# Kernel optimization log

Measured on AMD Instinct MI355X. Metric: run time of the kernel, lower is better.

Reference implementation:

```python
import jax, jax.numpy as jnp
import numpy as np
from jax.scipy.special import i0e

A = 10.0  # bessel concentration parameter (init kwarg a)


def setup_inputs() -> dict:
    key = jax.random.key(0)
    kx, ky = jax.random.split(key)
    x = jax.random.uniform(kx, (8192, 1), dtype=jnp.float32)
    y = jax.random.uniform(ky, (8192, 1), dtype=jnp.float32)
    return {"x": x, "y": y}


def reference(x, y):
    # K[i,j] = I0(2a*cos(pi*(x_i - y_j))) * exp(-2a)
    # Numerically stable form: I0(z)*exp(-2a) = i0e(z) * exp(|z| - 2a),
    # and |z| = |2a*cos(...)| <= 2a so the exponent is always <= 0.
    diff = x - y.T                      # [nx, ny]
    z = 2.0 * A * jnp.cos(jnp.pi * diff)
    return i0e(z) * jnp.exp(jnp.abs(z) - 2.0 * A)
```

## Files before the change

kernel.cpp:

```cpp
#include <hip/hip_runtime.h>
#include <hip/hip_bf16.h>


#define TWO_A 20.0f
#define EXP_NEG_2A 2.0611536224385578e-9f
#define LOG2E 1.4426950408889634f

__device__ __forceinline__ float bessel_elem(float xi, float yj) {
    float d = xi - yj;
#if __has_builtin(__builtin_amdgcn_cosf)
    float c = __builtin_amdgcn_cosf(0.5f * d);
#else
    float c = __cosf(3.14159265358979323846f * d);
#endif
    float az = TWO_A * fabsf(c);

    float t2 = az * (1.0f / 3.75f);
    t2 = t2 * t2;
    float ps = fmaf(t2, 0.0045813f, 0.0360768f);
    ps = fmaf(t2, ps, 0.2659732f);
    ps = fmaf(t2, ps, 1.2067492f);
    ps = fmaf(t2, ps, 3.0899424f);
    ps = fmaf(t2, ps, 3.5156229f);
    ps = fmaf(t2, ps, 1.0f);
    float k_small = ps * EXP_NEG_2A;

    float u = __fdividef(3.75f, az);
    float pl = fmaf(u, 0.00392377f, -0.01647633f);
    pl = fmaf(u, pl, 0.02635537f);
    pl = fmaf(u, pl, -0.02057706f);
    pl = fmaf(u, pl, 0.00916281f);
    pl = fmaf(u, pl, -0.00157565f);
    pl = fmaf(u, pl, 0.00225319f);
    pl = fmaf(u, pl, 0.01328592f);
    pl = fmaf(u, pl, 0.39894228f);
    float e = exp2f((az - TWO_A) * LOG2E);
    float k_large = pl * rsqrtf(az) * e;

    return (az < 3.75f) ? k_small : k_large;
}

__global__ __launch_bounds__(256) void bessel_kernel(
    const float* __restrict__ x, const float* __restrict__ y,
    float* __restrict__ out, int nx, int ny)
{
    const int i = blockIdx.y;
    const int j4 = (blockIdx.x * 256 + threadIdx.x) * 4;
    if (i >= nx || j4 >= ny) return;

    const float xi = x[i];
    float* orow = out + (size_t)i * (size_t)ny;

    if (j4 + 3 < ny) {
        float4 yv = *reinterpret_cast<const float4*>(y + j4);
        float4 o;
        o.x = bessel_elem(xi, yv.x);
        o.y = bessel_elem(xi, yv.y);
        o.z = bessel_elem(xi, yv.z);
        o.w = bessel_elem(xi, yv.w);
        *reinterpret_cast<float4*>(orow + j4) = o;
    } else {
        for (int j = j4; j < ny; ++j)
            orow[j] = bessel_elem(xi, y[j]);
    }
}

extern "C" void kernel_launch(void* const* d_in, const int* in_sizes, int n_in,
                              void* d_out, int out_size, void* d_ws, size_t ws_size,
                              hipStream_t stream) {
    const float* x = (const float*)d_in[0];
    const float* y = (const float*)d_in[1];
    float* out = (float*)d_out;
    const int nx = in_sizes[0];
    const int ny = in_sizes[1];

    const int jblocks = (ny + 4 * 256 - 1) / (4 * 256);
    dim3 grid(jblocks, nx);
    bessel_kernel<<<grid, 256, 0, stream>>>(x, y, out, nx, ny);
}
```

Measured before the change: 290.0 us.

## Replace piecewise Bessel approximation with single polynomial in cos squared

```diff
diff --git a/kernel.cpp b/kernel.cpp
--- a/kernel.cpp
+++ b/kernel.cpp
@@ -2,42 +2,40 @@
 #include <hip/hip_bf16.h>
 
 
-#define TWO_A 20.0f
-#define EXP_NEG_2A 2.0611536224385578e-9f
-#define LOG2E 1.4426950408889634f
+typedef float vfloat4 __attribute__((ext_vector_type(4)));
 
-__device__ __forceinline__ float bessel_elem(float xi, float yj) {
-    float d = xi - yj;
+__device__ __forceinline__ float bessel_u(float hd) {
 #if __has_builtin(__builtin_amdgcn_cosf)
-    float c = __builtin_amdgcn_cosf(0.5f * d);
+    float c = __builtin_amdgcn_cosf(hd);
 #else
-    float c = __cosf(3.14159265358979323846f * d);
+    float c = __cosf(6.283185307179586f * hd);
 #endif
-    float az = TWO_A * fabsf(c);
-
-    float t2 = az * (1.0f / 3.75f);
-    t2 = t2 * t2;
-    float ps = fmaf(t2, 0.0045813f, 0.0360768f);
-    ps = fmaf(t2, ps, 0.2659732f);
-    ps = fmaf(t2, ps, 1.2067492f);
-    ps = fmaf(t2, ps, 3.0899424f);
-    ps = fmaf(t2, ps, 3.5156229f);
-    ps = fmaf(t2, ps, 1.0f);
-    float k_small = ps * EXP_NEG_2A;
-
-    float u = __fdividef(3.75f, az);
-    float pl = fmaf(u, 0.00392377f, -0.01647633f);
-    pl = fmaf(u, pl, 0.02635537f);
-    pl = fmaf(u, pl, -0.02057706f);
-    pl = fmaf(u, pl, 0.00916281f);
-    pl = fmaf(u, pl, -0.00157565f);
-    pl = fmaf(u, pl, 0.00225319f);
-    pl = fmaf(u, pl, 0.01328592f);
-    pl = fmaf(u, pl, 0.39894228f);
-    float e = exp2f((az - TWO_A) * LOG2E);
-    float k_large = pl * rsqrtf(az) * e;
-
-    return (az < 3.75f) ? k_small : k_large;
+    float u = c * c;
+    float p =             3.08423e-8f;
+    p = fmaf(p, u, 1.63147e-7f);
+    p = fmaf(p, u, 7.89629e-7f);
+    p = fmaf(p, u, 3.48227e-6f);
+    p = fmaf(p, u, 1.39291e-5f);
+    p = fmaf(p, u, 5.02842e-5f);
+    p = fmaf(p, u, 1.62921e-4f);
+    p = fmaf(p, u, 4.70838e-4f);
+    p = fmaf(p, u, 1.20534e-3f);
+    p = fmaf(p, u, 2.71202e-3f);
+    p = fmaf(p, u, 5.31557e-3f);
+    p = fmaf(p, u, 8.98331e-3f);
+    p = fmaf(p, u, 1.29360e-2f);
+    p = fmaf(p, u, 1.56525e-2f);
+    p = fmaf(p, u, 1.56525e-2f);
+    p = fmaf(p, u, 1.26785e-2f);
+    p = fmaf(p, u, 8.11427e-3f);
+    p = fmaf(p, u, 3.97599e-3f);
+    p = fmaf(p, u, 1.43136e-3f);
+    p = fmaf(p, u, 3.57839e-4f);
+    p = fmaf(p, u, 5.72543e-5f);
+    p = fmaf(p, u, 5.15288e-6f);
+    p = fmaf(p, u, 2.06115e-7f);
+    p = fmaf(p, u, 2.06115362e-9f);
+    return p;
 }
 
 __global__ __launch_bounds__(256) void bessel_kernel(
@@ -45,23 +43,29 @@
     float* __restrict__ out, int nx, int ny)
 {
     const int i = blockIdx.y;
-    const int j4 = (blockIdx.x * 256 + threadIdx.x) * 4;
-    if (i >= nx || j4 >= ny) return;
+    const int j0 = (blockIdx.x * 256 + threadIdx.x) * 8;
+    if (i >= nx || j0 >= ny) return;
 
-    const float xi = x[i];
+    const float hx = 0.5f * x[i];
     float* orow = out + (size_t)i * (size_t)ny;
 
-    if (j4 + 3 < ny) {
-        float4 yv = *reinterpret_cast<const float4*>(y + j4);
-        float4 o;
-        o.x = bessel_elem(xi, yv.x);
-        o.y = bessel_elem(xi, yv.y);
-        o.z = bessel_elem(xi, yv.z);
-        o.w = bessel_elem(xi, yv.w);
-        *reinterpret_cast<float4*>(orow + j4) = o;
+    if (j0 + 7 < ny) {
+        vfloat4 ya = *reinterpret_cast<const vfloat4*>(y + j0);
+        vfloat4 yb = *reinterpret_cast<const vfloat4*>(y + j0 + 4);
+        vfloat4 oa, ob;
+        oa.x = bessel_u(hx - 0.5f * ya.x);
+        oa.y = bessel_u(hx - 0.5f * ya.y);
+        oa.z = bessel_u(hx - 0.5f * ya.z);
+        oa.w = bessel_u(hx - 0.5f * ya.w);
+        ob.x = bessel_u(hx - 0.5f * yb.x);
+        ob.y = bessel_u(hx - 0.5f * yb.y);
+        ob.z = bessel_u(hx - 0.5f * yb.z);
+        ob.w = bessel_u(hx - 0.5f * yb.w);
+        __builtin_nontemporal_store(oa, reinterpret_cast<vfloat4*>(orow + j0));
+        __builtin_nontemporal_store(ob, reinterpret_cast<vfloat4*>(orow + j0 + 4));
     } else {
-        for (int j = j4; j < ny; ++j)
-            orow[j] = bessel_elem(xi, y[j]);
+        for (int j = j0; j < ny; ++j)
+            orow[j] = bessel_u(hx - 0.5f * y[j]);
     }
 }
 
@@ -74,7 +78,7 @@
     const int nx = in_sizes[0];
     const int ny = in_sizes[1];
 
-    const int jblocks = (ny + 4 * 256 - 1) / (4 * 256);
+    const int jblocks = (ny + 8 * 256 - 1) / (8 * 256);
     dim3 grid(jblocks, nx);
     bessel_kernel<<<grid, 256, 0, stream>>>(x, y, out, nx, ny);
 }
```

After: 317.9 us. +9.6%, slower.
